# Optimization experiments

Measured on AMD Instinct MI355X. Metric: run time of the kernel, lower is better.

## Reference

```python
import jax, jax.numpy as jnp
import numpy as np

N = 100000
E = 3200000
IN_F = 256
OUT_F = 256


def setup_inputs() -> dict:
    key = jax.random.key(0)
    k1, k2, k3, k4, k5 = jax.random.split(key, 5)
    stdv = 1.0 / np.sqrt(OUT_F)
    x = jax.random.normal(k1, (N, IN_F), dtype=jnp.float32)
    edge_index = jax.random.randint(k2, (2, E), 0, N, dtype=jnp.int64)
    edge_weight = jax.random.uniform(k3, (E,), dtype=jnp.float32)
    weight = jax.random.uniform(k4, (IN_F, OUT_F), dtype=jnp.float32, minval=-stdv, maxval=stdv)
    bias = jax.random.uniform(k5, (OUT_F,), dtype=jnp.float32, minval=-stdv, maxval=stdv)
    return {"x": x, "edge_index": edge_index, "edge_weight": edge_weight,
            "weight": weight, "bias": bias}


def reference(x, edge_index, edge_weight, weight, bias):
    # Dense transform: [N, in] @ [in, out] -> [N, out]
    support = x @ weight
    row, col = edge_index[0], edge_index[1]
    # SpMM: out[row] += edge_weight * support[col]
    messages = edge_weight[:, None] * support[col]  # [E, out]
    output = jax.ops.segment_sum(messages, row, num_segments=N)  # [N, out]
    return output + bias
```

## Files before the change

### kernel.cpp

```cpp
#include <hip/hip_runtime.h>
#include <hip/hip_fp16.h>

#define IN_F 256
#define OUT_F 256
#define HALF_F 128
#define RPB_SHIFT 9
#define RPB (1 << RPB_SHIFT)
#define NBINS_MAX 256
#define TILE_E 4096
#define XS_PAD 40

using bf16x8 = __attribute__((ext_vector_type(8))) short;
using bf16x4 = __attribute__((ext_vector_type(4))) short;
using f32x4  = __attribute__((ext_vector_type(4))) float;
using ull    = unsigned long long;

__device__ inline short bf16rne(float f) {
    unsigned u = __float_as_uint(f);
    u = u + 0x7FFFu + ((u >> 16) & 1u);
    return (short)(u >> 16);
}
__device__ inline unsigned pack_half2(float a, float b) {
    __half2 h = __floats2half2_rn(a, b);
    return *reinterpret_cast<unsigned*>(&h);
}

__global__ __launch_bounds__(256) void convert_wt_kernel(
    const float* __restrict__ w, short* __restrict__ wt)
{
    const int idx = blockIdx.x * blockDim.x + threadIdx.x;
    const int c = idx >> 8, k = idx & 255;
    wt[(size_t)c * IN_F + k] = bf16rne(w[(size_t)k * OUT_F + c]);
}

__global__ __launch_bounds__(256) void mfma_gemm_kernel(
    const float* __restrict__ x, const short* __restrict__ wt,
    __half* __restrict__ supA, __half* __restrict__ supB, int M)
{
    __shared__ short xs[2][32][XS_PAD];

    const int t    = threadIdx.x;
    const int lane = t & 63;
    const int wid  = t >> 6;
    const int l15  = lane & 15;
    const int l4   = lane >> 4;
    const int rowbase = blockIdx.x * 32;
    const int cbase   = wid * 64;

    const int srow = t >> 3;
    const int sks  = (t & 7) * 4;
    int grow = rowbase + srow; if (grow > M - 1) grow = M - 1;
    const float* xsrc = x + (size_t)grow * IN_F + sks;

    f32x4 acc[2][4];
#pragma unroll
    for (int rt = 0; rt < 2; ++rt)
#pragma unroll
        for (int ct = 0; ct < 4; ++ct)
            acc[rt][ct] = (f32x4){0.f, 0.f, 0.f, 0.f};

    const short* wp[4];
#pragma unroll
    for (int ct = 0; ct < 4; ++ct)
        wp[ct] = wt + (size_t)(cbase + ct * 16 + l15) * IN_F + l4 * 8;

    {
        const float4 f = *(const float4*)xsrc;
        bf16x4 v;
        v[0] = bf16rne(f.x); v[1] = bf16rne(f.y);
        v[2] = bf16rne(f.z); v[3] = bf16rne(f.w);
        *(bf16x4*)&xs[0][srow][sks] = v;
    }
    __syncthreads();

#pragma unroll
    for (int k0 = 0; k0 < 8; ++k0) {
        const int cur = k0 & 1;

        float4 nf;
        if (k0 < 7) nf = *(const float4*)(xsrc + (k0 + 1) * 32);

        bf16x8 b[4];
#pragma unroll
        for (int ct = 0; ct < 4; ++ct)
            b[ct] = *(const bf16x8*)(wp[ct] + k0 * 32);

        bf16x8 a[2];
#pragma unroll
        for (int rt = 0; rt < 2; ++rt)
            a[rt] = *(const bf16x8*)&xs[cur][rt * 16 + l15][l4 * 8];

#pragma unroll
        for (int rt = 0; rt < 2; ++rt)
#pragma unroll
            for (int ct = 0; ct < 4; ++ct)
                acc[rt][ct] = __builtin_amdgcn_mfma_f32_16x16x32_bf16(
                    b[ct], a[rt], acc[rt][ct], 0, 0, 0);

        if (k0 < 7) {
            bf16x4 v;
            v[0] = bf16rne(nf.x); v[1] = bf16rne(nf.y);
            v[2] = bf16rne(nf.z); v[3] = bf16rne(nf.w);
            *(bf16x4*)&xs[cur ^ 1][srow][sks] = v;
        }
        __syncthreads();
    }

    __half* dst = (wid < 2) ? supA : supB;
    const int fbase = (wid & 1) * 64;
#pragma unroll
    for (int rt = 0; rt < 2; ++rt) {
        const int r = rowbase + rt * 16 + l15;
        if (r >= M) continue;
#pragma unroll
        for (int ct = 0; ct < 4; ++ct) {
            uint2 pk;
            pk.x = pack_half2(acc[rt][ct][0], acc[rt][ct][1]);
            pk.y = pack_half2(acc[rt][ct][2], acc[rt][ct][3]);
            *(uint2*)(dst + (size_t)r * HALF_F + fbase + ct * 16 + l4 * 4) = pk;
        }
    }
}

__global__ __launch_bounds__(256) void a1a_hist_kernel(
    const int* __restrict__ ei, int* __restrict__ thist, int E)
{
    __shared__ int hist[NBINS_MAX];
    const int tid = threadIdx.x;
    hist[tid] = 0;
    __syncthreads();
    const int base = blockIdx.x * TILE_E;
#pragma unroll
    for (int i = 0; i < TILE_E / 256; ++i) {
        const int e = base + i * 256 + tid;
        if (e < E)
            atomicAdd(&hist[__builtin_nontemporal_load(ei + e) >> RPB_SHIFT], 1);
    }
    __syncthreads();
    thist[(size_t)blockIdx.x * NBINS_MAX + tid] = hist[tid];
}

__global__ __launch_bounds__(256) void tile_scan_kernel(
    int* __restrict__ thist, int* __restrict__ btot, int T)
{
    const int b   = blockIdx.x;
    const int tid = threadIdx.x;
    __shared__ int s[256];
    int carry = 0;
    for (int c0 = 0; c0 < T; c0 += 256) {
        const int t = c0 + tid;
        const int v = (t < T) ? thist[(size_t)t * NBINS_MAX + b] : 0;
        s[tid] = v;
        __syncthreads();
        for (int d = 1; d < 256; d <<= 1) {
            const int u = (tid >= d) ? s[tid - d] : 0;
            __syncthreads();
            s[tid] += u;
            __syncthreads();
        }
        const int total = s[255];
        if (t < T) thist[(size_t)t * NBINS_MAX + b] = carry + s[tid] - v;
        carry += total;
        __syncthreads();
    }
    if (tid == 0) btot[b] = carry;
}

__global__ __launch_bounds__(NBINS_MAX) void bin_scan_kernel(
    const int* __restrict__ btot, int* __restrict__ bstart, int nbins)
{
    __shared__ int s[NBINS_MAX];
    const int tid = threadIdx.x;
    const int v = (tid < nbins) ? btot[tid] : 0;
    s[tid] = v;
    __syncthreads();
    for (int d = 1; d < NBINS_MAX; d <<= 1) {
        const int u = (tid >= d) ? s[tid - d] : 0;
        __syncthreads();
        s[tid] += u;
        __syncthreads();
    }
    bstart[tid] = s[tid] - v;
}

__global__ __launch_bounds__(256) void a1b_scatter_kernel(
    const int* __restrict__ ei, const float* __restrict__ ew,
    const int* __restrict__ bstart, const int* __restrict__ thist,
    ull* __restrict__ tscw, int E)
{
    __shared__ int hist[NBINS_MAX];
    __shared__ int rbase[NBINS_MAX];
    const int tid = threadIdx.x;
    hist[tid]  = 0;
    rbase[tid] = bstart[tid] + thist[(size_t)blockIdx.x * NBINS_MAX + tid];
    __syncthreads();
    const int base = blockIdx.x * TILE_E;
#pragma unroll
    for (int i = 0; i < TILE_E / 256; ++i) {
        const int e = base + i * 256 + tid;
        if (e < E) {
            const int      row = __builtin_nontemporal_load(ei + e);
            const int      col = __builtin_nontemporal_load(ei + E + e);
            const unsigned wb  = __builtin_nontemporal_load((const unsigned*)ew + e);
            const int b   = row >> RPB_SHIFT;
            const int rnk = atomicAdd(&hist[b], 1);
            tscw[rbase[b] + rnk] = ((ull)wb << 32) |
                                   ((unsigned)col << RPB_SHIFT) |
                                   (unsigned)(row & (RPB - 1));
        }
    }
}

__global__ __launch_bounds__(512) void a2_sort_kernel(
    const ull* __restrict__ tscw, const int* __restrict__ bstart,
    const int* __restrict__ btot, int* __restrict__ counts,
    int* __restrict__ cursor, unsigned* __restrict__ scw4, int M)
{
    const int b   = blockIdx.x;
    const int tid = threadIdx.x;
    const int n   = btot[b];
    const int s0  = bstart[b];

    __shared__ int hist[RPB];
    __shared__ int cur[RPB];
    __shared__ int s[RPB];

    hist[tid] = 0;
    __syncthreads();

    for (int i = tid; i < n; i += 512)
        atomicAdd(&hist[(int)(__builtin_nontemporal_load(tscw + s0 + i) & (RPB - 1))], 1);
    __syncthreads();

    const int own = hist[tid];
    s[tid] = own;
    __syncthreads();
    for (int d = 1; d < RPB; d <<= 1) {
        const int u = (tid >= d) ? s[tid - d] : 0;
        __syncthreads();
        s[tid] += u;
        __syncthreads();
    }
    const int excl = s[tid] - own;

    const int grow = (b << RPB_SHIFT) + tid;
    if (grow < M) { counts[grow] = own; cursor[grow] = s0 + excl; }
    cur[tid] = s0 + excl;
    __syncthreads();

    for (int i = tid; i < n; i += 512) {
        const ull en = __builtin_nontemporal_load(tscw + s0 + i);
        const int key = (int)(en & (RPB - 1));
        const unsigned col = (unsigned)((en >> RPB_SHIFT) & 0x1FFFFu);
        const float wf = __uint_as_float((unsigned)(en >> 32));
        const unsigned w15 = (unsigned)(wf * 32767.0f + 0.5f);
        const int pos = atomicAdd(&cur[key], 1);
        scw4[pos] = (w15 << 17) | col;
    }
}

__global__ __launch_bounds__(256) void pull_half_kernel(
    const int* __restrict__ counts, const int* __restrict__ cur_start,
    const unsigned* __restrict__ scw4, const __half* __restrict__ suph,
    const float* __restrict__ biash, float* __restrict__ outh, int M)
{
    const int wv  = blockIdx.x * 4 + (threadIdx.x >> 6);
    const int row = wv * 2 + ((threadIdx.x >> 5) & 1);
    if (row >= M) return;
    const int l = threadIdx.x & 31;

    const int cnt   = counts[row];
    const int start = cur_start[row];

    float4 acc = *(const float4*)(biash + l * 4);

#define GATHER_FMA_H(pe)                                                      \
    {                                                                         \
        const int   c  = (int)((pe) & 0x1FFFFu);                              \
        const float wj = (float)((pe) >> 17) * (1.0f / 32767.0f);             \
        const uint2 v = *(const uint2*)(suph + (size_t)c * HALF_F + l * 4);   \
        const float2 f0 = __half22float2(*(const __half2*)&v.x);              \
        const float2 f1 = __half22float2(*(const __half2*)&v.y);              \
        acc.x = fmaf(wj, f0.x, acc.x); acc.y = fmaf(wj, f0.y, acc.y);         \
        acc.z = fmaf(wj, f1.x, acc.z); acc.w = fmaf(wj, f1.y, acc.w);         \
    }

    for (int j0 = 0; j0 < cnt; j0 += 32) {
        unsigned pr = 0u;
        if (j0 + l < cnt)
            pr = __builtin_nontemporal_load(scw4 + start + j0 + l);
        const int m = min(32, cnt - j0);

        int j = 0;
        for (; j + 8 <= m; j += 8) {
            const unsigned p0 = __shfl(pr, j, 32),     p1 = __shfl(pr, j + 1, 32);
            const unsigned p2 = __shfl(pr, j + 2, 32), p3 = __shfl(pr, j + 3, 32);
            const unsigned p4 = __shfl(pr, j + 4, 32), p5 = __shfl(pr, j + 5, 32);
            const unsigned p6 = __shfl(pr, j + 6, 32), p7 = __shfl(pr, j + 7, 32);
            GATHER_FMA_H(p0); GATHER_FMA_H(p1); GATHER_FMA_H(p2); GATHER_FMA_H(p3);
            GATHER_FMA_H(p4); GATHER_FMA_H(p5); GATHER_FMA_H(p6); GATHER_FMA_H(p7);
        }
        for (; j < m; ++j) {
            const unsigned p = __shfl(pr, j, 32);
            GATHER_FMA_H(p);
        }
    }
#undef GATHER_FMA_H

    f32x4 o; o[0] = acc.x; o[1] = acc.y; o[2] = acc.z; o[3] = acc.w;
    __builtin_nontemporal_store(o, (f32x4*)(outh + (size_t)row * OUT_F + l * 4));
}

__global__ __launch_bounds__(256) void bias_init_kernel(
    float* __restrict__ out, const float* __restrict__ bias, int total4)
{
    const float4* b4 = (const float4*)bias;
    float4* o4 = (float4*)out;
    for (int i = blockIdx.x * blockDim.x + threadIdx.x; i < total4;
         i += gridDim.x * blockDim.x)
        o4[i] = b4[i & 63];
}

__global__ __launch_bounds__(256) void edge_scatter_kernel(
    const int* __restrict__ ei, const float* __restrict__ ew,
    const __half* __restrict__ supA, const __half* __restrict__ supB,
    float* __restrict__ out, int E)
{
    const int e = blockIdx.x * 4 + (threadIdx.x >> 6);
    if (e >= E) return;
    const int lane = threadIdx.x & 63;
    const int   row = ei[e];
    const int   col = ei[E + e];
    const float wgt = ew[e];
    const __half* src = (lane < 32) ? supA : supB;
    const int fl = (lane & 31) * 4;
    const uint2 v = *(const uint2*)(src + (size_t)col * HALF_F + fl);
    const float2 f0 = __half22float2(*(const __half2*)&v.x);
    const float2 f1 = __half22float2(*(const __half2*)&v.y);
    float* o = out + (size_t)row * OUT_F + (lane >> 5) * HALF_F + fl;
    unsafeAtomicAdd(o + 0, wgt * f0.x);
    unsafeAtomicAdd(o + 1, wgt * f0.y);
    unsafeAtomicAdd(o + 2, wgt * f1.x);
    unsafeAtomicAdd(o + 3, wgt * f1.y);
}

extern "C" void kernel_launch(void* const* d_in, const int* in_sizes, int n_in,
                              void* d_out, int out_size, void* d_ws, size_t ws_size,
                              hipStream_t stream)
{
    const float* x    = (const float*)d_in[0];
    const int*   ei   = (const int*)d_in[1];
    const float* ew   = (const float*)d_in[2];
    const float* w    = (const float*)d_in[3];
    const float* bias = (const float*)d_in[4];
    float* out = (float*)d_out;

    const int M = in_sizes[0] / IN_F;
    const int E = in_sizes[2];
    const int nbins = (M + RPB - 1) >> RPB_SHIFT;
    const int T     = (E + TILE_E - 1) / TILE_E;

    char* p = (char*)d_ws;
    const size_t suph_b   = (((size_t)M * HALF_F * sizeof(__half)) + 255) & ~255ull;
    const size_t counts_b = ((size_t)M * 4 + 255) & ~255ull;
    const size_t btot_b   = NBINS_MAX * 4;
    const size_t cstart_b = counts_b;
    const size_t bstart_b = NBINS_MAX * 4;
    const size_t thist_b  = (((size_t)T * NBINS_MAX * 4) + 255) & ~255ull;
    const size_t scw4_b   = ((size_t)E * 4 + 255) & ~255ull;
    const size_t tscw_b   = ((size_t)E * 8 + 255) & ~255ull;
    const size_t wt_b     = (size_t)IN_F * OUT_F * sizeof(short);
    const size_t need     = 2 * suph_b + counts_b + btot_b + cstart_b
                          + bstart_b + thist_b + scw4_b + tscw_b + wt_b;

    __half*   supA    = (__half*)p;            p += suph_b;
    __half*   supB    = (__half*)p;            p += suph_b;
    int*      counts  = (int*)p;               p += counts_b;
    int*      btot    = (int*)p;               p += btot_b;
    int*      cstart  = (int*)p;               p += cstart_b;
    int*      bstart  = (int*)p;               p += bstart_b;
    int*      thist   = (int*)p;               p += thist_b;
    unsigned* scw4    = (unsigned*)p;          p += scw4_b;
    ull*      tscw    = (ull*)p;               p += tscw_b;
    short*    wtb     = (short*)p;

    convert_wt_kernel<<<(IN_F * OUT_F) / 256, 256, 0, stream>>>(w, wtb);
    mfma_gemm_kernel<<<(M + 31) / 32, 256, 0, stream>>>(x, wtb, supA, supB, M);

    if (ws_size >= need) {
        a1a_hist_kernel<<<T, 256, 0, stream>>>(ei, thist, E);
        tile_scan_kernel<<<nbins, 256, 0, stream>>>(thist, btot, T);
        bin_scan_kernel<<<1, NBINS_MAX, 0, stream>>>(btot, bstart, nbins);
        a1b_scatter_kernel<<<T, 256, 0, stream>>>(ei, ew, bstart, thist, tscw, E);
        a2_sort_kernel<<<nbins, 512, 0, stream>>>(
            tscw, bstart, btot, counts, cstart, scw4, M);
        const int pblocks = ((M + 1) / 2 + 3) / 4;
        pull_half_kernel<<<pblocks, 256, 0, stream>>>(
            counts, cstart, scw4, supA, bias, out, M);
        pull_half_kernel<<<pblocks, 256, 0, stream>>>(
            counts, cstart, scw4, supB, bias + HALF_F, out + HALF_F, M);
    } else {
        const int total4 = M * OUT_F / 4;
        bias_init_kernel<<<2048, 256, 0, stream>>>(out, bias, total4);
        edge_scatter_kernel<<<(E + 3) / 4, 256, 0, stream>>>(ei, ew, supA, supB, out, E);
    }
}
```

Before: 408.4 us.

## Shard edges by source column range and pull with grid-synchronized cooperative kernel

The second sort pass now keys each row's edges by eight column shards (col>>14), so every row's edge list is grouped by source-feature region. A new cooperative pull kernel handles all rows concurrently, using persistent warps with register accumulators for up to 13 rows each. Shards are processed in lockstep with grid.sync between them, so the gathered support rows come from a small, cache-resident window of the feature table. This aims to raise L2/MALL hit rates on the random gather, at the cost of 16 grid-wide barriers, heavy register use for 13 float4 accumulators, and a fallback path when cooperative launch is unavailable.

```diff
diff --git a/kernel.cpp b/kernel.cpp
--- a/kernel.cpp
+++ b/kernel.cpp
@@ -1,5 +1,8 @@
 #include <hip/hip_runtime.h>
 #include <hip/hip_fp16.h>
+#include <hip/hip_cooperative_groups.h>
+
+namespace cg = cooperative_groups;
 
 #define IN_F 256
 #define OUT_F 256
@@ -9,6 +12,11 @@
 #define NBINS_MAX 256
 #define TILE_E 4096
 #define XS_PAD 40
+#define SHARD_SHIFT 14
+#define NKEY (RPB * 8)
+#define PULL_BLOCKS 1024
+#define SLOTS (PULL_BLOCKS * 8)
+#define MAX_IT 13
 
 using bf16x8 = __attribute__((ext_vector_type(8))) short;
 using bf16x4 = __attribute__((ext_vector_type(4))) short;
@@ -167,7 +175,8 @@
 }
 
 __global__ __launch_bounds__(NBINS_MAX) void bin_scan_kernel(
-    const int* __restrict__ btot, int* __restrict__ bstart, int nbins)
+    const int* __restrict__ btot, int* __restrict__ bstart,
+    int* __restrict__ pstart, int nbins)
 {
     __shared__ int s[NBINS_MAX];
     const int tid = threadIdx.x;
@@ -181,6 +190,7 @@
         __syncthreads();
     }
     bstart[tid] = s[tid] - v;
+    if (tid == 0) pstart[(size_t)nbins * NKEY] = s[NBINS_MAX - 1];
 }
 
 __global__ __launch_bounds__(256) void a1b_scatter_kernel(
@@ -213,64 +223,139 @@
 
 __global__ __launch_bounds__(512) void a2_sort_kernel(
     const ull* __restrict__ tscw, const int* __restrict__ bstart,
-    const int* __restrict__ btot, int* __restrict__ counts,
-    int* __restrict__ cursor, unsigned* __restrict__ scw4, int M)
+    const int* __restrict__ btot, int* __restrict__ pstart,
+    unsigned* __restrict__ scw4)
 {
     const int b   = blockIdx.x;
     const int tid = threadIdx.x;
     const int n   = btot[b];
     const int s0  = bstart[b];
 
-    __shared__ int hist[RPB];
-    __shared__ int cur[RPB];
-    __shared__ int s[RPB];
-
-    hist[tid] = 0;
-    __syncthreads();
-
-    for (int i = tid; i < n; i += 512)
-        atomicAdd(&hist[(int)(__builtin_nontemporal_load(tscw + s0 + i) & (RPB - 1))], 1);
-    __syncthreads();
-
-    const int own = hist[tid];
-    s[tid] = own;
-    __syncthreads();
-    for (int d = 1; d < RPB; d <<= 1) {
-        const int u = (tid >= d) ? s[tid - d] : 0;
-        __syncthreads();
-        s[tid] += u;
-        __syncthreads();
-    }
-    const int excl = s[tid] - own;
-
-    const int grow = (b << RPB_SHIFT) + tid;
-    if (grow < M) { counts[grow] = own; cursor[grow] = s0 + excl; }
-    cur[tid] = s0 + excl;
+    __shared__ int h[NKEY];
+    __shared__ int s[512];
+
+#pragma unroll
+    for (int k = 0; k < NKEY / 512; ++k) h[tid + k * 512] = 0;
     __syncthreads();
 
     for (int i = tid; i < n; i += 512) {
         const ull en = __builtin_nontemporal_load(tscw + s0 + i);
-        const int key = (int)(en & (RPB - 1));
+        const int key = ((int)(en & (RPB - 1)) << 3) |
+                        (int)((en >> (RPB_SHIFT + SHARD_SHIFT)) & 7u);
+        atomicAdd(&h[key], 1);
+    }
+    __syncthreads();
+
+    int loc[8];
+    int run = 0;
+#pragma unroll
+    for (int k = 0; k < 8; ++k) { loc[k] = h[tid * 8 + k]; run += loc[k]; }
+    s[tid] = run;
+    __syncthreads();
+    for (int d = 1; d < 512; d <<= 1) {
+        const int u = (tid >= d) ? s[tid - d] : 0;
+        __syncthreads();
+        s[tid] += u;
+        __syncthreads();
+    }
+    int accum = s[tid] - run;
+    const size_t g0 = (size_t)b * NKEY + (size_t)tid * 8;
+#pragma unroll
+    for (int k = 0; k < 8; ++k) {
+        pstart[g0 + k] = s0 + accum;
+        loc[k] = s0 + accum;
+        accum += h[tid * 8 + k];
+    }
+    __syncthreads();
+#pragma unroll
+    for (int k = 0; k < 8; ++k) h[tid * 8 + k] = loc[k];
+    __syncthreads();
+
+    for (int i = tid; i < n; i += 512) {
+        const ull en = __builtin_nontemporal_load(tscw + s0 + i);
+        const int key = ((int)(en & (RPB - 1)) << 3) |
+                        (int)((en >> (RPB_SHIFT + SHARD_SHIFT)) & 7u);
         const unsigned col = (unsigned)((en >> RPB_SHIFT) & 0x1FFFFu);
         const float wf = __uint_as_float((unsigned)(en >> 32));
         const unsigned w15 = (unsigned)(wf * 32767.0f + 0.5f);
-        const int pos = atomicAdd(&cur[key], 1);
+        const int pos = atomicAdd(&h[key], 1);
         scw4[pos] = (w15 << 17) | col;
     }
 }
 
+__global__ __launch_bounds__(256, 4) void pull_coop_kernel(
+    const int* __restrict__ pstart, const unsigned* __restrict__ scw4,
+    const __half* __restrict__ supA, const __half* __restrict__ supB,
+    const float* __restrict__ bias, float* __restrict__ out, int M)
+{
+    cg::grid_group grid = cg::this_grid();
+    const int gw2 = (blockIdx.x * 256 + threadIdx.x) >> 5;
+    const int l   = threadIdx.x & 31;
+
+#pragma unroll
+    for (int half = 0; half < 2; ++half) {
+        const __half* suph = half ? supB : supA;
+        const float4 bv = *(const float4*)(bias + half * HALF_F + l * 4);
+
+        float4 acc[MAX_IT];
+#pragma unroll
+        for (int it = 0; it < MAX_IT; ++it) acc[it] = bv;
+
+        for (int sh = 0; sh < 8; ++sh) {
+#pragma unroll
+            for (int it = 0; it < MAX_IT; ++it) {
+                const int row = it * SLOTS + gw2;
+                if (row < M) {
+                    const int st = pstart[(size_t)row * 8 + sh];
+                    const int en = pstart[(size_t)row * 8 + sh + 1];
+                    for (int j0 = st; j0 < en; j0 += 32) {
+                        unsigned pr = 0u;
+                        if (j0 + l < en) pr = scw4[j0 + l];
+                        const int m = min(32, en - j0);
+                        for (int j = 0; j < m; ++j) {
+                            const unsigned pe = __shfl(pr, j, 32);
+                            const int   c  = (int)(pe & 0x1FFFFu);
+                            const float wj = (float)(pe >> 17) * (1.0f / 32767.0f);
+                            const uint2 v = *(const uint2*)(suph + (size_t)c * HALF_F + l * 4);
+                            const float2 f0 = __half22float2(*(const __half2*)&v.x);
+                            const float2 f1 = __half22float2(*(const __half2*)&v.y);
+                            acc[it].x = fmaf(wj, f0.x, acc[it].x);
+                            acc[it].y = fmaf(wj, f0.y, acc[it].y);
+                            acc[it].z = fmaf(wj, f1.x, acc[it].z);
+                            acc[it].w = fmaf(wj, f1.y, acc[it].w);
+                        }
+                    }
+                }
+            }
+            grid.sync();
+        }
+
+#pragma unroll
+        for (int it = 0; it < MAX_IT; ++it) {
+            const int row = it * SLOTS + gw2;
+            if (row < M) {
+                f32x4 o;
+                o[0] = acc[it].x; o[1] = acc[it].y;
+                o[2] = acc[it].z; o[3] = acc[it].w;
+                __builtin_nontemporal_store(
+                    o, (f32x4*)(out + (size_t)row * OUT_F + half * HALF_F + l * 4));
+            }
+        }
+    }
+}
+
 __global__ __launch_bounds__(256) void pull_half_kernel(
-    const int* __restrict__ counts, const int* __restrict__ cur_start,
-    const unsigned* __restrict__ scw4, const __half* __restrict__ suph,
-    const float* __restrict__ biash, float* __restrict__ outh, int M)
+    const int* __restrict__ pstart, const unsigned* __restrict__ scw4,
+    const __half* __restrict__ suph, const float* __restrict__ biash,
+    float* __restrict__ outh, int M)
 {
     const int wv  = blockIdx.x * 4 + (threadIdx.x >> 6);
     const int row = wv * 2 + ((threadIdx.x >> 5) & 1);
     if (row >= M) return;
     const int l = threadIdx.x & 31;
 
-    const int cnt   = counts[row];
-    const int start = cur_start[row];
+    const int start = pstart[(size_t)row * 8];
+    const int cnt   = pstart[(size_t)row * 8 + 8] - start;
 
     float4 acc = *(const float4*)(biash + l * 4);
 
@@ -362,24 +447,22 @@
 
     char* p = (char*)d_ws;
     const size_t suph_b   = (((size_t)M * HALF_F * sizeof(__half)) + 255) & ~255ull;
-    const size_t counts_b = ((size_t)M * 4 + 255) & ~255ull;
     const size_t btot_b   = NBINS_MAX * 4;
-    const size_t cstart_b = counts_b;
     const size_t bstart_b = NBINS_MAX * 4;
     const size_t thist_b  = (((size_t)T * NBINS_MAX * 4) + 255) & ~255ull;
+    const size_t pstart_b = (((size_t)nbins * NKEY + 256) * 4 + 255) & ~255ull;
     const size_t scw4_b   = ((size_t)E * 4 + 255) & ~255ull;
     const size_t tscw_b   = ((size_t)E * 8 + 255) & ~255ull;
     const size_t wt_b     = (size_t)IN_F * OUT_F * sizeof(short);
-    const size_t need     = 2 * suph_b + counts_b + btot_b + cstart_b
-                          + bstart_b + thist_b + scw4_b + tscw_b + wt_b;
+    const size_t need     = 2 * suph_b + btot_b + bstart_b + thist_b
+                          + pstart_b + scw4_b + tscw_b + wt_b;
 
     __half*   supA    = (__half*)p;            p += suph_b;
     __half*   supB    = (__half*)p;            p += suph_b;
-    int*      counts  = (int*)p;               p += counts_b;
     int*      btot    = (int*)p;               p += btot_b;
-    int*      cstart  = (int*)p;               p += cstart_b;
     int*      bstart  = (int*)p;               p += bstart_b;
     int*      thist   = (int*)p;               p += thist_b;
+    int*      pstart  = (int*)p;               p += pstart_b;
     unsigned* scw4    = (unsigned*)p;          p += scw4_b;
     ull*      tscw    = (ull*)p;               p += tscw_b;
     short*    wtb     = (short*)p;
@@ -390,15 +473,36 @@
     if (ws_size >= need) {
         a1a_hist_kernel<<<T, 256, 0, stream>>>(ei, thist, E);
         tile_scan_kernel<<<nbins, 256, 0, stream>>>(thist, btot, T);
-        bin_scan_kernel<<<1, NBINS_MAX, 0, stream>>>(btot, bstart, nbins);
+        bin_scan_kernel<<<1, NBINS_MAX, 0, stream>>>(btot, bstart, pstart, nbins);
         a1b_scatter_kernel<<<T, 256, 0, stream>>>(ei, ew, bstart, thist, tscw, E);
-        a2_sort_kernel<<<nbins, 512, 0, stream>>>(
-            tscw, bstart, btot, counts, cstart, scw4, M);
-        const int pblocks = ((M + 1) / 2 + 3) / 4;
-        pull_half_kernel<<<pblocks, 256, 0, stream>>>(
-            counts, cstart, scw4, supA, bias, out, M);
-        pull_half_kernel<<<pblocks, 256, 0, stream>>>(
-            counts, cstart, scw4, supB, bias + HALF_F, out + HALF_F, M);
+        a2_sort_kernel<<<nbins, 512, 0, stream>>>(tscw, bstart, btot, pstart, scw4);
+
+        bool coop_done = false;
+        const bool rows_fit = ((M + SLOTS - 1) / SLOTS) <= MAX_IT;
+        if (rows_fit) {
+            int dev = 0;
+            (void)hipGetDevice(&dev);
+            int coopAttr = 0, numCU = 0, maxB = 0;
+            (void)hipDeviceGetAttribute(&coopAttr, hipDeviceAttributeCooperativeLaunch, dev);
+            (void)hipDeviceGetAttribute(&numCU, hipDeviceAttributeMultiprocessorCount, dev);
+            hipError_t occ = hipOccupancyMaxActiveBlocksPerMultiprocessor(
+                &maxB, pull_coop_kernel, 256, 0);
+            if (coopAttr && occ == hipSuccess && (long long)maxB * numCU >= PULL_BLOCKS) {
+                void* kargs[] = {(void*)&pstart, (void*)&scw4, (void*)&supA,
+                                 (void*)&supB, (void*)&bias, (void*)&out, (void*)&M};
+                hipError_t lerr = hipLaunchCooperativeKernel(
+                    (void*)pull_coop_kernel, dim3(PULL_BLOCKS), dim3(256),
+                    kargs, 0, stream);
+                coop_done = (lerr == hipSuccess);
+            }
+        }
+        if (!coop_done) {
+            const int pblocks = ((M + 1) / 2 + 3) / 4;
+            pull_half_kernel<<<pblocks, 256, 0, stream>>>(
+                pstart, scw4, supA, bias, out, M);
+            pull_half_kernel<<<pblocks, 256, 0, stream>>>(
+                pstart, scw4, supB, bias + HALF_F, out + HALF_F, M);
+        }
     } else {
         const int total4 = M * OUT_F / 4;
         bias_init_kernel<<<2048, 256, 0, stream>>>(out, bias, total4);
```

Measured after the change: 405.3 us. About the same (-0.7%).
